# Optimization experiments

Hardware: AMD Instinct MI355X
Metric: run time of the kernel (lower is better)

Reference implementation:

```python
import jax, jax.numpy as jnp
import numpy as np


def binarize_ste(W):
    # sign binarization with straight-through estimator:
    # forward = sign(W) (zeros mapped to +1, standard BNN convention),
    # backward = identity.
    s = jnp.where(W >= 0, 1.0, -1.0).astype(W.dtype)
    return W + jax.lax.stop_gradient(s - W)


def setup_inputs() -> dict:
    key = jax.random.key(0)
    k1, k2 = jax.random.split(key)
    B, N_IN, N_UNITS = 4096, 4096, 4096
    x = jax.random.normal(k1, (B, N_IN), dtype=jnp.float32)
    W = jax.random.normal(k2, (N_IN, N_UNITS), dtype=jnp.float32) * 0.1  # truncated_normal(stddev=0.1) analog
    b = jnp.zeros((N_UNITS,), dtype=jnp.float32)  # constant_initializer(0.0)
    return {"x": x, "W": W, "b": b}


def reference(x, W, b):
    bin_w = binarize_ste(W)           # [n_in, n_units], values in {-1, +1}
    out = x @ bin_w + b               # dense GEMM + bias
    return jax.nn.relu(out)           # act
```

## Files before the change

### kernel.cpp

```cpp
#include <hip/hip_runtime.h>
#include <hip/hip_bf16.h>

typedef unsigned short u16;
typedef signed char i8;
typedef __attribute__((ext_vector_type(4))) int   int4v;
typedef __attribute__((ext_vector_type(4))) float f32x4;

#define GLOBAL_AS __attribute__((address_space(1)))
#define LDS_AS    __attribute__((address_space(3)))

__device__ __forceinline__ void gload_lds16(const void* g, void* l) {
    __builtin_amdgcn_global_load_lds((const GLOBAL_AS unsigned int*)g,
                                     (LDS_AS unsigned int*)l, 16, 0, 0);
}

__global__ __launch_bounds__(256) void quant_x_kernel(const float* __restrict__ X,
                                                      i8* __restrict__ Xq,
                                                      float* __restrict__ inv_s) {
    const int row = blockIdx.x;
    const int t   = threadIdx.x;
    const float4* src = (const float4*)(X + (size_t)row * 4096 + t * 16);
    float4 v0 = src[0], v1 = src[1], v2 = src[2], v3 = src[3];
    float vals[16] = {v0.x, v0.y, v0.z, v0.w, v1.x, v1.y, v1.z, v1.w,
                      v2.x, v2.y, v2.z, v2.w, v3.x, v3.y, v3.z, v3.w};
    float m = 0.f;
#pragma unroll
    for (int j = 0; j < 16; ++j) m = fmaxf(m, fabsf(vals[j]));
#pragma unroll
    for (int off = 32; off; off >>= 1) m = fmaxf(m, __shfl_xor(m, off));
    __shared__ float sm[4];
    if ((t & 63) == 0) sm[t >> 6] = m;
    __syncthreads();
    m = fmaxf(fmaxf(sm[0], sm[1]), fmaxf(sm[2], sm[3]));
    const float s = (m > 0.f) ? 127.0f / m : 0.f;
    uint4 packed;
    unsigned int* pw = (unsigned int*)&packed;
#pragma unroll
    for (int g = 0; g < 4; ++g) {
        unsigned int wd = 0;
#pragma unroll
        for (int j = 0; j < 4; ++j) {
            int q = (int)rintf(vals[g * 4 + j] * s);
            wd |= ((unsigned int)(q & 255)) << (8 * j);
        }
        pw[g] = wd;
    }
    ((uint4*)(Xq + (size_t)row * 4096))[t] = packed;
    if (t == 0) inv_s[row] = m * (1.0f / 127.0f);
}

__global__ __launch_bounds__(256) void conv_w_kernel(const float* __restrict__ W,
                                                     i8* __restrict__ Wt) {
    __shared__ __attribute__((aligned(16))) i8 tile[64][80];
    const int t  = threadIdx.x;
    const int k0 = (blockIdx.x & 63) * 64;
    const int n0 = (blockIdx.x >> 6) * 64;
#pragma unroll
    for (int i = 0; i < 4; ++i) {
        const int r = i * 16 + (t >> 4);
        const int c = (t & 15) * 4;
        float4 v = *(const float4*)&W[(size_t)(k0 + r) * 4096 + n0 + c];
        tile[c + 0][r] = (v.x >= 0.f) ? 1 : -1;
        tile[c + 1][r] = (v.y >= 0.f) ? 1 : -1;
        tile[c + 2][r] = (v.z >= 0.f) ? 1 : -1;
        tile[c + 3][r] = (v.w >= 0.f) ? 1 : -1;
    }
    __syncthreads();
    const int r = t >> 2;
    const int c = (t & 3) * 16;
    *(int4*)&Wt[(size_t)(n0 + r) * 4096 + k0 + c] = *(const int4*)&tile[r][c];
}


#define BAR()        __builtin_amdgcn_s_barrier()
#define LGKM0M()     asm volatile("s_waitcnt lgkmcnt(0)" ::: "memory")
#define WAIT_VM4()   asm volatile("s_waitcnt vmcnt(4)" ::: "memory")

#define STAGE_TILE(base, koff)                                                      \
    do {                                                                            \
        gload_lds16(AsrcT + (koff),         lds + (base) + wA);                     \
        gload_lds16(AsrcT + 65536 + (koff), lds + (base) + wA + 1024);              \
        gload_lds16(BsrcT + (koff),         lds + (base) + 16384 + wA);             \
        gload_lds16(BsrcT + 65536 + (koff), lds + (base) + 16384 + wA + 1024);      \
    } while (0)

__global__ __launch_bounds__(512, 2) void gemm_bin_kernel(const i8* __restrict__ A,
                                                          const i8* __restrict__ Bt,
                                                          const float* __restrict__ bias,
                                                          const float* __restrict__ inv_s,
                                                          float* __restrict__ C) {
    __shared__ __attribute__((aligned(1024))) char lds[98304];

    const int bid = blockIdx.x;
    const int swz = (bid & 7) * 32 + (bid >> 3);
    const int bm  = swz >> 4;
    const int bn  = swz & 15;

    const int tid = threadIdx.x;
    const int w   = tid >> 6;
    const int l   = tid & 63;
    const int wm  = w >> 2;
    const int wn  = w & 3;

    const int lin8 = (l & 7) ^ (l >> 3);
    const int sr2  = (l >> 3) * 2 + (lin8 >> 2);
    const int sc   = (lin8 & 3) * 16;
    const char* AsrcT = (const char*)A  + (size_t)(bm * 256 + 32 * w + sr2) * 4096 + sc;
    const char* BsrcT = (const char*)Bt + (size_t)(bn * 256 + 32 * w + sr2) * 4096 + sc;
    const int wA = w * 2048;

    const int rsl  = ((l >> 4) + 4 * (l & 1)) ^ ((l >> 1) & 7);
    const int a_rd = wm * 8192 + ((l & 15) >> 1) * 128 + rsl * 16;
    const int b_rd = 16384 + wn * 4096 + ((l & 15) >> 1) * 128 + rsl * 16;

    int4v acc[8][4] = {};
    int4v af[8], bf[4];

    STAGE_TILE(0, 0);
    STAGE_TILE(32768, 64);
    WAIT_VM4();
    BAR();

    int rb = 0;
    int sb = 65536;
    for (int t = 0; t < 64; ++t) {
        const int koff2 = ((t + 2) & 63) * 64;

        STAGE_TILE(sb, koff2);

#pragma unroll
        for (int mi = 0; mi < 8; ++mi)
            af[mi] = *(const int4v*)(lds + rb + a_rd + mi * 1024);
#pragma unroll
        for (int ni = 0; ni < 4; ++ni)
            bf[ni] = *(const int4v*)(lds + rb + b_rd + ni * 1024);

        __builtin_amdgcn_s_setprio(1);
#pragma unroll
        for (int mi = 0; mi < 8; ++mi)
#pragma unroll
            for (int ni = 0; ni < 4; ++ni)
                acc[mi][ni] = __builtin_amdgcn_mfma_i32_16x16x64_i8(af[mi], bf[ni],
                                                                    acc[mi][ni], 0, 0, 0);
        __builtin_amdgcn_s_setprio(0);

        WAIT_VM4();
        LGKM0M();
        BAR();
        sb = rb;
        rb = (rb == 65536) ? 0 : rb + 32768;
    }
    asm volatile("s_waitcnt vmcnt(0) lgkmcnt(0)" ::: "memory");

    const int col0 = bn * 256 + wn * 64 + (l & 15);
    const int row0 = bm * 256 + wm * 128 + ((l >> 4) << 2);
    float bn4[4];
#pragma unroll
    for (int n = 0; n < 4; ++n) bn4[n] = bias[col0 + n * 16];
#pragma unroll
    for (int m = 0; m < 8; ++m) {
#pragma unroll
        for (int r = 0; r < 4; ++r) {
            const int   grow = row0 + m * 16 + r;
            const float ivs  = inv_s[grow];
#pragma unroll
            for (int n = 0; n < 4; ++n) {
                const float v = (float)acc[m][n][r] * ivs + bn4[n];
                C[(size_t)grow * 4096 + (col0 + n * 16)] = v > 0.f ? v : 0.f;
            }
        }
    }
}

__global__ __launch_bounds__(256) void fallback_kernel(const float* __restrict__ X,
                                                       const float* __restrict__ W,
                                                       const float* __restrict__ b,
                                                       float* __restrict__ out) {
    __shared__ float xs[16][16];
    __shared__ float ws[16][17];
    const int row = blockIdx.y * 16 + threadIdx.y;
    const int col = blockIdx.x * 16 + threadIdx.x;
    float acc = 0.f;
    for (int k0 = 0; k0 < 4096; k0 += 16) {
        xs[threadIdx.y][threadIdx.x] = X[(size_t)row * 4096 + k0 + threadIdx.x];
        float w = W[(size_t)(k0 + threadIdx.y) * 4096 + col];
        ws[threadIdx.y][threadIdx.x] = (w >= 0.f) ? 1.f : -1.f;
        __syncthreads();
#pragma unroll
        for (int kk = 0; kk < 16; ++kk) acc += xs[threadIdx.y][kk] * ws[kk][threadIdx.x];
        __syncthreads();
    }
    const float v = acc + b[col];
    out[(size_t)row * 4096 + col] = v > 0.f ? v : 0.f;
}

extern "C" void kernel_launch(void* const* d_in, const int* in_sizes, int n_in,
                              void* d_out, int out_size, void* d_ws, size_t ws_size,
                              hipStream_t stream) {
    const float* x = (const float*)d_in[0];
    const float* W = (const float*)d_in[1];
    const float* b = (const float*)d_in[2];
    float* out = (float*)d_out;

    const size_t need = (size_t)32 * 1024 * 1024 + 64 * 1024;
    if (ws_size < need) {
        fallback_kernel<<<dim3(256, 256), dim3(16, 16), 0, stream>>>(x, W, b, out);
        return;
    }

    i8*    Xq  = (i8*)d_ws;
    i8*    Wt  = Xq + (size_t)4096 * 4096;
    float* ivs = (float*)(Xq + (size_t)2 * 4096 * 4096);

    quant_x_kernel<<<dim3(4096), dim3(256), 0, stream>>>(x, Xq, ivs);
    conv_w_kernel<<<dim3(4096), dim3(256), 0, stream>>>(W, Wt);
    gemm_bin_kernel<<<dim3(256), dim3(512), 0, stream>>>(Xq, Wt, b, ivs, out);
}
```

Measured before the change: 97.60 us.

## Load A fragments directly from global into registers, stage only B through LDS

The A operand is no longer staged through LDS. Each wave loads its own A fragments straight from global memory into a double-buffered register set one k-step ahead, while B keeps its LDS staging, now with four smaller buffers. The loop is unrolled by four so buffer offsets and the A register ping-pong become constants. This cuts LDS traffic and LDS footprint, at the cost of redundant global/L2 reads of A across the four N-waves, more VGPR pressure, and uncoalesced 16-byte strided global loads.

```diff
diff --git a/kernel.cpp b/kernel.cpp
--- a/kernel.cpp
+++ b/kernel.cpp
@@ -74,14 +74,33 @@
 
 #define BAR()        __builtin_amdgcn_s_barrier()
 #define LGKM0M()     asm volatile("s_waitcnt lgkmcnt(0)" ::: "memory")
-#define WAIT_VM4()   asm volatile("s_waitcnt vmcnt(4)" ::: "memory")
-
-#define STAGE_TILE(base, koff)                                                      \
+#define WAIT_VM10()  asm volatile("s_waitcnt vmcnt(10)" ::: "memory")
+#define WAIT_VM2()   asm volatile("s_waitcnt vmcnt(2)" ::: "memory")
+
+#define STAGE_B(base, koff)                                                         \
     do {                                                                            \
-        gload_lds16(AsrcT + (koff),         lds + (base) + wA);                     \
-        gload_lds16(AsrcT + 65536 + (koff), lds + (base) + wA + 1024);              \
-        gload_lds16(BsrcT + (koff),         lds + (base) + 16384 + wA);             \
-        gload_lds16(BsrcT + 65536 + (koff), lds + (base) + 16384 + wA + 1024);      \
+        gload_lds16(BsrcT + (koff),         lds + (base) + wB);                     \
+        gload_lds16(BsrcT + 65536 + (koff), lds + (base) + wB + 1024);              \
+    } while (0)
+
+#define BODY(tt, RB, SB, AC, AN)                                                    \
+    do {                                                                            \
+        const int kA = (((tt) + 1) & 63) * 64;                                      \
+        const int kB = (((tt) + 2) & 63) * 64;                                      \
+        _Pragma("unroll") for (int mi = 0; mi < 8; ++mi)                            \
+            AN[mi] = *(const int4v*)(Agl + aoff[mi] + kA);                          \
+        STAGE_B(SB, kB);                                                            \
+        _Pragma("unroll") for (int ni = 0; ni < 4; ++ni)                            \
+            bf[ni] = *(const int4v*)(lds + (RB) + b_rd + ni * 1024);                \
+        __builtin_amdgcn_s_setprio(1);                                              \
+        _Pragma("unroll") for (int mi = 0; mi < 8; ++mi)                            \
+        _Pragma("unroll") for (int ni = 0; ni < 4; ++ni)                            \
+            acc[mi][ni] = __builtin_amdgcn_mfma_i32_16x16x64_i8(AC[mi], bf[ni],     \
+                                                                acc[mi][ni], 0, 0, 0); \
+        __builtin_amdgcn_s_setprio(0);                                              \
+        WAIT_VM10();                                                                \
+        LGKM0M();                                                                   \
+        BAR();                                                                      \
     } while (0)
 
 __global__ __launch_bounds__(512, 2) void gemm_bin_kernel(const i8* __restrict__ A,
@@ -89,7 +108,7 @@
                                                           const float* __restrict__ bias,
                                                           const float* __restrict__ inv_s,
                                                           float* __restrict__ C) {
-    __shared__ __attribute__((aligned(1024))) char lds[98304];
+    __shared__ __attribute__((aligned(1024))) char lds[65536];
 
     const int bid = blockIdx.x;
     const int swz = (bid & 7) * 32 + (bid >> 3);
@@ -102,53 +121,39 @@
     const int wm  = w >> 2;
     const int wn  = w & 3;
 
+    const char* Agl = (const char*)A + (size_t)(bm * 256) * 4096;
+    int aoff[8];
+#pragma unroll
+    for (int mi = 0; mi < 8; ++mi)
+        aoff[mi] = (wm * 128 + mi * 16 + (l & 15)) * 4096 + (l >> 4) * 16;
+
     const int lin8 = (l & 7) ^ (l >> 3);
     const int sr2  = (l >> 3) * 2 + (lin8 >> 2);
     const int sc   = (lin8 & 3) * 16;
-    const char* AsrcT = (const char*)A  + (size_t)(bm * 256 + 32 * w + sr2) * 4096 + sc;
     const char* BsrcT = (const char*)Bt + (size_t)(bn * 256 + 32 * w + sr2) * 4096 + sc;
-    const int wA = w * 2048;
+    const int wB = w * 2048;
 
     const int rsl  = ((l >> 4) + 4 * (l & 1)) ^ ((l >> 1) & 7);
-    const int a_rd = wm * 8192 + ((l & 15) >> 1) * 128 + rsl * 16;
-    const int b_rd = 16384 + wn * 4096 + ((l & 15) >> 1) * 128 + rsl * 16;
+    const int b_rd = wn * 4096 + ((l & 15) >> 1) * 128 + rsl * 16;
 
     int4v acc[8][4] = {};
-    int4v af[8], bf[4];
-
-    STAGE_TILE(0, 0);
-    STAGE_TILE(32768, 64);
-    WAIT_VM4();
+    int4v aX[8], aY[8];
+    int4v bf[4];
+
+#pragma unroll
+    for (int mi = 0; mi < 8; ++mi)
+        aX[mi] = *(const int4v*)(Agl + aoff[mi]);
+    STAGE_B(0, 0);
+    STAGE_B(16384, 64);
+    WAIT_VM2();
     BAR();
 
-    int rb = 0;
-    int sb = 65536;
-    for (int t = 0; t < 64; ++t) {
-        const int koff2 = ((t + 2) & 63) * 64;
-
-        STAGE_TILE(sb, koff2);
-
-#pragma unroll
-        for (int mi = 0; mi < 8; ++mi)
-            af[mi] = *(const int4v*)(lds + rb + a_rd + mi * 1024);
-#pragma unroll
-        for (int ni = 0; ni < 4; ++ni)
-            bf[ni] = *(const int4v*)(lds + rb + b_rd + ni * 1024);
-
-        __builtin_amdgcn_s_setprio(1);
-#pragma unroll
-        for (int mi = 0; mi < 8; ++mi)
-#pragma unroll
-            for (int ni = 0; ni < 4; ++ni)
-                acc[mi][ni] = __builtin_amdgcn_mfma_i32_16x16x64_i8(af[mi], bf[ni],
-                                                                    acc[mi][ni], 0, 0, 0);
-        __builtin_amdgcn_s_setprio(0);
-
-        WAIT_VM4();
-        LGKM0M();
-        BAR();
-        sb = rb;
-        rb = (rb == 65536) ? 0 : rb + 32768;
+    for (int m4 = 0; m4 < 16; ++m4) {
+        const int t4 = m4 * 4;
+        BODY(t4 + 0,     0, 32768, aX, aY);
+        BODY(t4 + 1, 16384, 49152, aY, aX);
+        BODY(t4 + 2, 32768,     0, aX, aY);
+        BODY(t4 + 3, 49152, 16384, aY, aX);
     }
     asm volatile("s_waitcnt vmcnt(0) lgkmcnt(0)" ::: "memory");
 
```

Result: slower. 192.2 us (+97.0%).

## Switch int8 GEMM to 32x32x32 MFMA with 4 waves and 128x128 warp tiles

Applied to the files above, without the earlier changes.

The int8 GEMM moves from 16x16x64 MFMA with 8 waves (128x64 per wave) to 32x32x32 MFMA with 4 waves (128x128 per wave). Each wave now stages twice as many rows per tile, and the vmcnt threshold and LDS read swizzle change to match. The aim is to raise MFMA throughput and cut LDS fragment reads per output element by using the larger instruction and bigger per-wave tiles. In exchange each workgroup has fewer waves and more accumulator registers (256 VGPRs of acc), which may hurt latency hiding.

```diff
diff --git a/kernel.cpp b/kernel.cpp
--- a/kernel.cpp
+++ b/kernel.cpp
@@ -3,8 +3,8 @@
 
 typedef unsigned short u16;
 typedef signed char i8;
-typedef __attribute__((ext_vector_type(4))) int   int4v;
-typedef __attribute__((ext_vector_type(4))) float f32x4;
+typedef __attribute__((ext_vector_type(4)))  int int4v;
+typedef __attribute__((ext_vector_type(16))) int int16v;
 
 #define GLOBAL_AS __attribute__((address_space(1)))
 #define LDS_AS    __attribute__((address_space(3)))
@@ -74,17 +74,17 @@
 
 #define BAR()        __builtin_amdgcn_s_barrier()
 #define LGKM0M()     asm volatile("s_waitcnt lgkmcnt(0)" ::: "memory")
-#define WAIT_VM4()   asm volatile("s_waitcnt vmcnt(4)" ::: "memory")
+#define WAIT_VM8()   asm volatile("s_waitcnt vmcnt(8)" ::: "memory")
 
 #define STAGE_TILE(base, koff)                                                      \
     do {                                                                            \
-        gload_lds16(AsrcT + (koff),         lds + (base) + wA);                     \
-        gload_lds16(AsrcT + 65536 + (koff), lds + (base) + wA + 1024);              \
-        gload_lds16(BsrcT + (koff),         lds + (base) + 16384 + wA);             \
-        gload_lds16(BsrcT + 65536 + (koff), lds + (base) + 16384 + wA + 1024);      \
+        _Pragma("unroll") for (int j = 0; j < 4; ++j)                               \
+            gload_lds16(AsrcT + j * 65536 + (koff), lds + (base) + wS + j * 1024);  \
+        _Pragma("unroll") for (int j = 0; j < 4; ++j)                               \
+            gload_lds16(BsrcT + j * 65536 + (koff), lds + (base) + 16384 + wS + j * 1024); \
     } while (0)
 
-__global__ __launch_bounds__(512, 2) void gemm_bin_kernel(const i8* __restrict__ A,
+__global__ __launch_bounds__(256, 1) void gemm_bin_kernel(const i8* __restrict__ A,
                                                           const i8* __restrict__ Bt,
                                                           const float* __restrict__ bias,
                                                           const float* __restrict__ inv_s,
@@ -99,26 +99,27 @@
     const int tid = threadIdx.x;
     const int w   = tid >> 6;
     const int l   = tid & 63;
-    const int wm  = w >> 2;
-    const int wn  = w & 3;
+    const int wm  = w >> 1;
+    const int wn  = w & 1;
 
     const int lin8 = (l & 7) ^ (l >> 3);
     const int sr2  = (l >> 3) * 2 + (lin8 >> 2);
     const int sc   = (lin8 & 3) * 16;
-    const char* AsrcT = (const char*)A  + (size_t)(bm * 256 + 32 * w + sr2) * 4096 + sc;
-    const char* BsrcT = (const char*)Bt + (size_t)(bn * 256 + 32 * w + sr2) * 4096 + sc;
-    const int wA = w * 2048;
-
-    const int rsl  = ((l >> 4) + 4 * (l & 1)) ^ ((l >> 1) & 7);
-    const int a_rd = wm * 8192 + ((l & 15) >> 1) * 128 + rsl * 16;
-    const int b_rd = 16384 + wn * 4096 + ((l & 15) >> 1) * 128 + rsl * 16;
-
-    int4v acc[8][4] = {};
-    int4v af[8], bf[4];
+    const char* AsrcT = (const char*)A  + (size_t)(bm * 256 + w * 64 + sr2) * 4096 + sc;
+    const char* BsrcT = (const char*)Bt + (size_t)(bn * 256 + w * 64 + sr2) * 4096 + sc;
+    const int wS = w * 4096;
+
+    const int rd_sl    = ((((l >> 5) + 4 * (l & 1)) ^ ((l >> 1) & 7)) << 4);
+    const int row_part = ((l >> 1) & 15) * 128;
+    const int a_rd = wm * 8192 + row_part + rd_sl;
+    const int b_rd = 16384 + wn * 8192 + row_part + rd_sl;
+
+    int16v acc[4][4] = {};
+    int4v  af[4], bf[4];
 
     STAGE_TILE(0, 0);
     STAGE_TILE(32768, 64);
-    WAIT_VM4();
+    WAIT_VM8();
     BAR();
 
     int rb = 0;
@@ -129,22 +130,24 @@
         STAGE_TILE(sb, koff2);
 
 #pragma unroll
-        for (int mi = 0; mi < 8; ++mi)
-            af[mi] = *(const int4v*)(lds + rb + a_rd + mi * 1024);
-#pragma unroll
-        for (int ni = 0; ni < 4; ++ni)
-            bf[ni] = *(const int4v*)(lds + rb + b_rd + ni * 1024);
-
-        __builtin_amdgcn_s_setprio(1);
-#pragma unroll
-        for (int mi = 0; mi < 8; ++mi)
-#pragma unroll
-            for (int ni = 0; ni < 4; ++ni)
-                acc[mi][ni] = __builtin_amdgcn_mfma_i32_16x16x64_i8(af[mi], bf[ni],
-                                                                    acc[mi][ni], 0, 0, 0);
-        __builtin_amdgcn_s_setprio(0);
-
-        WAIT_VM4();
+        for (int ks = 0; ks < 2; ++ks) {
+#pragma unroll
+            for (int mi = 0; mi < 4; ++mi)
+                af[mi] = *(const int4v*)(lds + ((rb + a_rd + mi * 2048) ^ (ks * 32)));
+#pragma unroll
+            for (int nj = 0; nj < 4; ++nj)
+                bf[nj] = *(const int4v*)(lds + ((rb + b_rd + nj * 2048) ^ (ks * 32)));
+            __builtin_amdgcn_s_setprio(1);
+#pragma unroll
+            for (int mi = 0; mi < 4; ++mi)
+#pragma unroll
+                for (int nj = 0; nj < 4; ++nj)
+                    acc[mi][nj] = __builtin_amdgcn_mfma_i32_32x32x32_i8(af[mi], bf[nj],
+                                                                        acc[mi][nj], 0, 0, 0);
+            __builtin_amdgcn_s_setprio(0);
+        }
+
+        WAIT_VM8();
         LGKM0M();
         BAR();
         sb = rb;
@@ -152,21 +155,22 @@
     }
     asm volatile("s_waitcnt vmcnt(0) lgkmcnt(0)" ::: "memory");
 
-    const int col0 = bn * 256 + wn * 64 + (l & 15);
-    const int row0 = bm * 256 + wm * 128 + ((l >> 4) << 2);
-    float bn4[4];
-#pragma unroll
-    for (int n = 0; n < 4; ++n) bn4[n] = bias[col0 + n * 16];
-#pragma unroll
-    for (int m = 0; m < 8; ++m) {
-#pragma unroll
-        for (int r = 0; r < 4; ++r) {
-            const int   grow = row0 + m * 16 + r;
+    const int col0 = bn * 256 + wn * 128 + (l & 31);
+    const int row0 = bm * 256 + wm * 128 + 4 * (l >> 5);
+    float bi4[4];
+#pragma unroll
+    for (int nj = 0; nj < 4; ++nj) bi4[nj] = bias[col0 + nj * 32];
+#pragma unroll
+    for (int mi = 0; mi < 4; ++mi) {
+#pragma unroll
+        for (int reg = 0; reg < 16; ++reg) {
+            const int   grow = row0 + mi * 32 + (reg & 3) + 8 * (reg >> 2);
             const float ivs  = inv_s[grow];
-#pragma unroll
-            for (int n = 0; n < 4; ++n) {
-                const float v = (float)acc[m][n][r] * ivs + bn4[n];
-                C[(size_t)grow * 4096 + (col0 + n * 16)] = v > 0.f ? v : 0.f;
+            float* crow = C + (size_t)grow * 4096 + col0;
+#pragma unroll
+            for (int nj = 0; nj < 4; ++nj) {
+                const float v = (float)acc[mi][nj][reg] * ivs + bi4[nj];
+                crow[nj * 32] = v > 0.f ? v : 0.f;
             }
         }
     }
@@ -214,5 +218,5 @@
 
     quant_x_kernel<<<dim3(4096), dim3(256), 0, stream>>>(x, Xq, ivs);
     conv_w_kernel<<<dim3(4096), dim3(256), 0, stream>>>(W, Wt);
-    gemm_bin_kernel<<<dim3(256), dim3(512), 0, stream>>>(Xq, Wt, b, ivs, out);
-}
+    gemm_bin_kernel<<<dim3(256), dim3(256), 0, stream>>>(Xq, Wt, b, ivs, out);
+}
```

Result: slower. 105.9 us (+8.5%).

## Ping-pong wave groups over a four-stage LDS ring in binary GEMM

Applied to the files above, without the earlier changes.

Splits the eight waves into two groups that alternate between an LDS-fragment-read-plus-staging phase and an MFMA phase, separated by block barriers. One group's memory work overlaps the other's matrix math. LDS grows to a four-buffer ring with three tiles prefetched up front, so global loads run further ahead. The cost is an extra barrier per iteration and tighter cross-wave scheduling that depends on correct vmcnt accounting.

```diff
diff --git a/kernel.cpp b/kernel.cpp
--- a/kernel.cpp
+++ b/kernel.cpp
@@ -75,6 +75,7 @@
 #define BAR()        __builtin_amdgcn_s_barrier()
 #define LGKM0M()     asm volatile("s_waitcnt lgkmcnt(0)" ::: "memory")
 #define WAIT_VM4()   asm volatile("s_waitcnt vmcnt(4)" ::: "memory")
+#define WAIT_VM8()   asm volatile("s_waitcnt vmcnt(8)" ::: "memory")
 
 #define STAGE_TILE(base, koff)                                                      \
     do {                                                                            \
@@ -84,12 +85,30 @@
         gload_lds16(BsrcT + 65536 + (koff), lds + (base) + 16384 + wA + 1024);      \
     } while (0)
 
+#define READ_FRAGS(base)                                                            \
+    do {                                                                            \
+        _Pragma("unroll") for (int mi = 0; mi < 8; ++mi)                            \
+            af[mi] = *(const int4v*)(lds + (base) + a_rd + mi * 1024);              \
+        _Pragma("unroll") for (int ni = 0; ni < 4; ++ni)                            \
+            bf[ni] = *(const int4v*)(lds + (base) + b_rd + ni * 1024);              \
+    } while (0)
+
+#define MFMA_ALL()                                                                  \
+    do {                                                                            \
+        __builtin_amdgcn_s_setprio(1);                                              \
+        _Pragma("unroll") for (int mi = 0; mi < 8; ++mi)                            \
+        _Pragma("unroll") for (int ni = 0; ni < 4; ++ni)                            \
+            acc[mi][ni] = __builtin_amdgcn_mfma_i32_16x16x64_i8(af[mi], bf[ni],     \
+                                                                acc[mi][ni], 0, 0, 0); \
+        __builtin_amdgcn_s_setprio(0);                                              \
+    } while (0)
+
 __global__ __launch_bounds__(512, 2) void gemm_bin_kernel(const i8* __restrict__ A,
                                                           const i8* __restrict__ Bt,
                                                           const float* __restrict__ bias,
                                                           const float* __restrict__ inv_s,
                                                           float* __restrict__ C) {
-    __shared__ __attribute__((aligned(1024))) char lds[98304];
+    __shared__ __attribute__((aligned(1024))) char lds[131072];
 
     const int bid = blockIdx.x;
     const int swz = (bid & 7) * 32 + (bid >> 3);
@@ -101,6 +120,7 @@
     const int l   = tid & 63;
     const int wm  = w >> 2;
     const int wn  = w & 3;
+    const bool isE = (w < 4);
 
     const int lin8 = (l & 7) ^ (l >> 3);
     const int sr2  = (l >> 3) * 2 + (lin8 >> 2);
@@ -118,37 +138,37 @@
 
     STAGE_TILE(0, 0);
     STAGE_TILE(32768, 64);
-    WAIT_VM4();
+    STAGE_TILE(65536, 128);
+    WAIT_VM8();
     BAR();
-
-    int rb = 0;
-    int sb = 65536;
+    if (isE) { READ_FRAGS(0); LGKM0M(); }
+    BAR();
+
     for (int t = 0; t < 64; ++t) {
-        const int koff2 = ((t + 2) & 63) * 64;
-
-        STAGE_TILE(sb, koff2);
-
-#pragma unroll
-        for (int mi = 0; mi < 8; ++mi)
-            af[mi] = *(const int4v*)(lds + rb + a_rd + mi * 1024);
-#pragma unroll
-        for (int ni = 0; ni < 4; ++ni)
-            bf[ni] = *(const int4v*)(lds + rb + b_rd + ni * 1024);
-
-        __builtin_amdgcn_s_setprio(1);
-#pragma unroll
-        for (int mi = 0; mi < 8; ++mi)
-#pragma unroll
-            for (int ni = 0; ni < 4; ++ni)
-                acc[mi][ni] = __builtin_amdgcn_mfma_i32_16x16x64_i8(af[mi], bf[ni],
-                                                                    acc[mi][ni], 0, 0, 0);
-        __builtin_amdgcn_s_setprio(0);
-
-        WAIT_VM4();
-        LGKM0M();
+        const int bufR  = (t & 3) * 32768;
+        const int bufR1 = ((t + 1) & 3) * 32768;
+        const int bufS3 = ((t + 3) & 3) * 32768;
+        const int ko3   = ((t + 3) & 63) * 64;
+
+        if (!isE) {
+            WAIT_VM4();
+            READ_FRAGS(bufR);
+            STAGE_TILE(bufS3, ko3);
+            LGKM0M();
+        } else {
+            MFMA_ALL();
+        }
         BAR();
-        sb = rb;
-        rb = (rb == 65536) ? 0 : rb + 32768;
+
+        if (isE) {
+            WAIT_VM4();
+            READ_FRAGS(bufR1);
+            STAGE_TILE(bufS3, ko3);
+            LGKM0M();
+        } else {
+            MFMA_ALL();
+        }
+        BAR();
     }
     asm volatile("s_waitcnt vmcnt(0) lgkmcnt(0)" ::: "memory");
 
```

Measured after the change: 95.58 us. 1.02x faster.
